# Performance work log

Hardware: AMD Instinct MI355X
Metric: run time of the kernel (lower is better)

Reference implementation:

```python
import jax, jax.numpy as jnp
import numpy as np

LN_EPS = 1e-5
B, N, D, V = 2048, 8, 1024, 4096


def setup_inputs() -> dict:
    key = jax.random.key(0)
    k1, k2, k3, k4 = jax.random.split(key, 4)
    return {
        "input_embedding": jax.random.normal(k1, (B, D), dtype=jnp.float32),
        "features": jax.random.randint(k2, (B, N), 0, V, dtype=jnp.int64),
        "embed_tables": jax.random.normal(k3, (N, V, D), dtype=jnp.float32) * 0.02,
        "W_pred": jax.random.normal(k4, (N, D, V), dtype=jnp.float32) * 0.02,
        "b_pred": jnp.zeros((N, V), dtype=jnp.float32),
        "ln_gamma": jnp.ones((D,), dtype=jnp.float32),
        "ln_beta": jnp.zeros((D,), dtype=jnp.float32),
    }


def reference(input_embedding, features, embed_tables, W_pred, b_pred, ln_gamma, ln_beta):
    # Per-feature embedding lookup: embed_tables[n, features[b,n]] -> [B, N, D]
    feat_emb = embed_tables[jnp.arange(N)[None, :], features]
    # Stack input embedding in front: [B, N+1, D]
    embeddings = jnp.concatenate([input_embedding[:, None, :], feat_emb], axis=1)
    # Original: triu(diag=1) mask-multiply-sum then [:, 1:, :].
    # masked_sums[:, t] = sum_{s < t} emb[:, s]; slicing t=1..N == inclusive cumsum
    # over the first N positions.
    masked_sums = jnp.cumsum(embeddings, axis=1)[:, :-1, :]  # [B, N, D]
    # LayerNorm over last dim
    mu = jnp.mean(masked_sums, axis=-1, keepdims=True)
    var = jnp.var(masked_sums, axis=-1, keepdims=True)
    h = (masked_sums - mu) / jnp.sqrt(var + LN_EPS) * ln_gamma + ln_beta
    # Exact (erf) GELU, matching nn.GELU default
    h = jax.nn.gelu(h, approximate=False)
    # Per-feature predictor heads as one batched GEMM: [B, N, V]
    logits = jnp.einsum("bnd,ndv->bnv", h, W_pred) + b_pred
    return logits
```

## Files before the change

kernel.cpp:

```cpp
#include <hip/hip_runtime.h>
#include <hip/hip_bf16.h>

#define B_ 2048
#define N_ 8
#define D_ 1024
#define V_ 4096
#define LN_EPS_ 1e-5f

typedef __bf16 bf16x8 __attribute__((ext_vector_type(8)));
typedef float f32x4 __attribute__((ext_vector_type(4)));

#define GLB(p) ((const __attribute__((address_space(1))) void*)(p))
#define LDSP(p) ((__attribute__((address_space(3))) void*)(p))

static __device__ __forceinline__ unsigned short f2bf(float x) {
    union { float f; unsigned int u; } v;
    v.f = x;
    unsigned int r = v.u + 0x7fffu + ((v.u >> 16) & 1u);
    return (unsigned short)(r >> 16);
}

__global__ __launch_bounds__(256) void prep(const float* __restrict__ ie,
                                            const int* __restrict__ feats,
                                            const float* __restrict__ emb,
                                            const float* __restrict__ gamma,
                                            const float* __restrict__ beta,
                                            const float* __restrict__ W,
                                            unsigned short* __restrict__ H,
                                            unsigned short* __restrict__ Wt) {
    const int bid = blockIdx.x;
    const int t = threadIdx.x;

    if (bid >= 2048) {
        __shared__ unsigned short tile[64][65];
        const int w  = bid - 2048;
        const int v0 = (w & 63) * 64;
        const int d0 = ((w >> 6) & 15) * 64;
        const int n  = w >> 10;
        const int tx = t & 15, ty = t >> 4;
#pragma unroll
        for (int i = 0; i < 4; ++i) {
            const int d = ty + i * 16;
            const float4 w4 = *(const float4*)&W[((size_t)n * D_ + d0 + d) * V_ + v0 + tx * 4];
            tile[d][tx * 4 + 0] = f2bf(w4.x);
            tile[d][tx * 4 + 1] = f2bf(w4.y);
            tile[d][tx * 4 + 2] = f2bf(w4.z);
            tile[d][tx * 4 + 3] = f2bf(w4.w);
        }
        __syncthreads();
#pragma unroll
        for (int i = 0; i < 4; ++i) {
            const int v = ty + i * 16;
            ushort4 pk;
            pk.x = tile[tx * 4 + 0][v];
            pk.y = tile[tx * 4 + 1][v];
            pk.z = tile[tx * 4 + 2][v];
            pk.w = tile[tx * 4 + 3][v];
            *reinterpret_cast<ushort4*>(&Wt[((size_t)n * V_ + v0 + v) * D_ + d0 + tx * 4]) = pk;
        }
    } else {
        __shared__ float redS[4], redQ[4];
        const int b = bid;
        const int d0 = t * 4;
        const int lane = t & 63, wid = t >> 6;

        float4 s  = *(const float4*)&ie[(size_t)b * D_ + d0];
        const float4 g4 = *(const float4*)&gamma[d0];
        const float4 be4 = *(const float4*)&beta[d0];

        int fc[N_];
#pragma unroll
        for (int n = 0; n < N_; ++n) fc[n] = feats[b * N_ + n];

#pragma unroll
        for (int n = 0; n < N_; ++n) {
            float ls = s.x + s.y + s.z + s.w;
            float lq = s.x * s.x + s.y * s.y + s.z * s.z + s.w * s.w;
#pragma unroll
            for (int off = 32; off > 0; off >>= 1) {
                ls += __shfl_down(ls, off, 64);
                lq += __shfl_down(lq, off, 64);
            }
            if (lane == 0) { redS[wid] = ls; redQ[wid] = lq; }
            __syncthreads();
            const float tot  = redS[0] + redS[1] + redS[2] + redS[3];
            const float totq = redQ[0] + redQ[1] + redQ[2] + redQ[3];
            __syncthreads();

            const float mu   = tot * (1.0f / D_);
            const float var  = totq * (1.0f / D_) - mu * mu;
            const float rstd = rsqrtf(var + LN_EPS_);

            float h0 = (s.x - mu) * rstd * g4.x + be4.x;
            float h1 = (s.y - mu) * rstd * g4.y + be4.y;
            float h2 = (s.z - mu) * rstd * g4.z + be4.z;
            float h3 = (s.w - mu) * rstd * g4.w + be4.w;
            h0 = 0.5f * h0 * (1.0f + erff(h0 * 0.70710678f));
            h1 = 0.5f * h1 * (1.0f + erff(h1 * 0.70710678f));
            h2 = 0.5f * h2 * (1.0f + erff(h2 * 0.70710678f));
            h3 = 0.5f * h3 * (1.0f + erff(h3 * 0.70710678f));

            ushort4 pk;
            pk.x = f2bf(h0); pk.y = f2bf(h1); pk.z = f2bf(h2); pk.w = f2bf(h3);
            *reinterpret_cast<ushort4*>(&H[((size_t)n * B_ + b) * D_ + d0]) = pk;

            const float4 e = *(const float4*)&emb[((size_t)n * V_ + fc[n]) * (size_t)D_ + d0];
            s.x += e.x; s.y += e.y; s.z += e.z; s.w += e.w;
        }
    }
}

#define MF(a, b, c) __builtin_amdgcn_mfma_f32_16x16x32_bf16((a), (b), (c), 0, 0, 0)

#define STG_A(u, kt, bb) __builtin_amdgcn_global_load_lds( \
    GLB(Ab + (size_t)((u) * 64 + srow) * D_ + (kt) + gsl), \
    LDSP(lds + (bb) + (u) * 8192 + t * 16), 16, 0, 0)
#define STG_B(u, kt, bb) __builtin_amdgcn_global_load_lds( \
    GLB(Bb + (size_t)((u) * 64 + srow) * D_ + (kt) + gsl), \
    LDSP(lds + (bb) + 32768 + (u) * 8192 + t * 16), 16, 0, 0)

#define RD_A(i, ks, bb) (*(const bf16x8*)(lds + (bb) + ((i) >> 1) * 8192 + \
    (((i) & 1) * 32 + wr * 16 + lrow) * 128 + ((((ks) * 4 + lkq) ^ sw) * 16)))
#define RD_B(j, ks, bb) (*(const bf16x8*)(lds + (bb) + 32768 + wc * 8192 + \
    ((j) * 16 + lrow) * 128 + ((((ks) * 4 + lkq) ^ sw) * 16)))

#define QUADP(i0, i1) \
    _Pragma("unroll") for (int j = 0; j < 4; ++j) { \
        acc[i0][j] = MF(A00, Bf[j][0], acc[i0][j]); \
        acc[i0][j] = MF(A01, Bf[j][1], acc[i0][j]); \
        acc[i1][j] = MF(A10, Bf[j][0], acc[i1][j]); \
        acc[i1][j] = MF(A11, Bf[j][1], acc[i1][j]); \
    }

#define TILE(KT, bc, bn) { \
    bf16x8 Bf[4][2]; \
    asm volatile("s_waitcnt vmcnt(3)" ::: "memory"); \
    __builtin_amdgcn_s_barrier(); \
    _Pragma("unroll") for (int j = 0; j < 4; ++j) { Bf[j][0] = RD_B(j, 0, bc); Bf[j][1] = RD_B(j, 1, bc); } \
    { bf16x8 A00 = RD_A(0, 0, bc), A01 = RD_A(0, 1, bc), A10 = RD_A(1, 0, bc), A11 = RD_A(1, 1, bc); \
      STG_B(0, (KT) + 64, bn); STG_B(1, (KT) + 64, bn); \
      __builtin_amdgcn_s_setprio(1); QUADP(0, 1); __builtin_amdgcn_s_setprio(0); } \
    __builtin_amdgcn_s_barrier(); \
    asm volatile("s_waitcnt vmcnt(4)" ::: "memory"); \
    __builtin_amdgcn_s_barrier(); \
    { bf16x8 A00 = RD_A(2, 0, bc), A01 = RD_A(2, 1, bc), A10 = RD_A(3, 0, bc), A11 = RD_A(3, 1, bc); \
      STG_B(2, (KT) + 64, bn); STG_B(3, (KT) + 64, bn); \
      __builtin_amdgcn_s_setprio(1); QUADP(2, 3); __builtin_amdgcn_s_setprio(0); } \
    __builtin_amdgcn_s_barrier(); \
    asm volatile("s_waitcnt vmcnt(4)" ::: "memory"); \
    __builtin_amdgcn_s_barrier(); \
    { bf16x8 A00 = RD_A(4, 0, bc), A01 = RD_A(4, 1, bc), A10 = RD_A(5, 0, bc), A11 = RD_A(5, 1, bc); \
      STG_A(0, (KT) + 64, bn); STG_A(1, (KT) + 64, bn); \
      __builtin_amdgcn_s_setprio(1); QUADP(4, 5); __builtin_amdgcn_s_setprio(0); } \
    __builtin_amdgcn_s_barrier(); \
    asm volatile("s_waitcnt vmcnt(6)" ::: "memory"); \
    __builtin_amdgcn_s_barrier(); \
    { bf16x8 A00 = RD_A(6, 0, bc), A01 = RD_A(6, 1, bc), A10 = RD_A(7, 0, bc), A11 = RD_A(7, 1, bc); \
      STG_A(2, (KT) + 64, bn); STG_A(3, (KT) + 64, bn); \
      __builtin_amdgcn_s_setprio(1); QUADP(6, 7); __builtin_amdgcn_s_setprio(0); } \
    __builtin_amdgcn_s_barrier(); \
}

#define TILE_LAST(bc) { \
    bf16x8 Bf[4][2]; \
    asm volatile("s_waitcnt vmcnt(3)" ::: "memory"); \
    __builtin_amdgcn_s_barrier(); \
    _Pragma("unroll") for (int j = 0; j < 4; ++j) { Bf[j][0] = RD_B(j, 0, bc); Bf[j][1] = RD_B(j, 1, bc); } \
    { bf16x8 A00 = RD_A(0, 0, bc), A01 = RD_A(0, 1, bc), A10 = RD_A(1, 0, bc), A11 = RD_A(1, 1, bc); \
      __builtin_amdgcn_s_setprio(1); QUADP(0, 1); __builtin_amdgcn_s_setprio(0); } \
    __builtin_amdgcn_s_barrier(); \
    asm volatile("s_waitcnt vmcnt(2)" ::: "memory"); \
    __builtin_amdgcn_s_barrier(); \
    { bf16x8 A00 = RD_A(2, 0, bc), A01 = RD_A(2, 1, bc), A10 = RD_A(3, 0, bc), A11 = RD_A(3, 1, bc); \
      __builtin_amdgcn_s_setprio(1); QUADP(2, 3); __builtin_amdgcn_s_setprio(0); } \
    __builtin_amdgcn_s_barrier(); \
    asm volatile("s_waitcnt vmcnt(1)" ::: "memory"); \
    __builtin_amdgcn_s_barrier(); \
    { bf16x8 A00 = RD_A(4, 0, bc), A01 = RD_A(4, 1, bc), A10 = RD_A(5, 0, bc), A11 = RD_A(5, 1, bc); \
      __builtin_amdgcn_s_setprio(1); QUADP(4, 5); __builtin_amdgcn_s_setprio(0); } \
    __builtin_amdgcn_s_barrier(); \
    asm volatile("s_waitcnt vmcnt(0)" ::: "memory"); \
    __builtin_amdgcn_s_barrier(); \
    { bf16x8 A00 = RD_A(6, 0, bc), A01 = RD_A(6, 1, bc), A10 = RD_A(7, 0, bc), A11 = RD_A(7, 1, bc); \
      __builtin_amdgcn_s_setprio(1); QUADP(6, 7); __builtin_amdgcn_s_setprio(0); } \
}

__global__ __launch_bounds__(512, 2) void gemm8(const unsigned short* __restrict__ H,
                                                const unsigned short* __restrict__ Wt,
                                                const float* __restrict__ bp,
                                                float* __restrict__ out) {
    extern __shared__ char lds[];
    const int vt = blockIdx.x, mt = blockIdx.y, n = blockIdx.z;
    const int t = threadIdx.x;
    const int wid = t >> 6, lane = t & 63;
    const int wr = wid >> 2, wc = wid & 3;

    const unsigned short* Ab = H  + ((size_t)n * B_ + (size_t)mt * 256) * D_;
    const unsigned short* Bb = Wt + ((size_t)n * V_ + (size_t)vt * 256) * D_;

    const int srow = t >> 3;
    const int gsl  = ((t & 7) ^ (srow & 7)) * 8;
    const int lrow = lane & 15;
    const int lkq  = lane >> 4;
    const int sw   = lane & 7;

    const int col = lane & 15;
    float bias[4];
#pragma unroll
    for (int j = 0; j < 4; ++j)
        bias[j] = bp[(size_t)n * V_ + vt * 256 + wc * 64 + j * 16 + col];
    asm volatile("s_waitcnt vmcnt(0)" ::: "memory");
    __builtin_amdgcn_sched_barrier(0);

    f32x4 acc[8][4] = {};

    STG_B(0, 0, 0); STG_B(1, 0, 0); STG_B(2, 0, 0); STG_B(3, 0, 0);
    STG_A(0, 0, 0); STG_A(1, 0, 0); STG_A(2, 0, 0); STG_A(3, 0, 0);

    int kt = 0;
#pragma unroll 1
    for (int it = 0; it < 7; ++it) {
        TILE(kt, 0, 65536); kt += 64;
        TILE(kt, 65536, 0); kt += 64;
    }
    TILE(kt, 0, 65536);
    TILE_LAST(65536);

    const int rg  = (lane >> 4) * 4;
    const int gc0 = vt * 256 + wc * 64 + col;
#pragma unroll
    for (int i = 0; i < 8; ++i) {
        const int row = mt * 256 + i * 32 + wr * 16 + rg;
#pragma unroll
        for (int j = 0; j < 4; ++j) {
            const int gcol = gc0 + j * 16;
#pragma unroll
            for (int r = 0; r < 4; ++r) {
                out[((size_t)(row + r) * N_ + n) * V_ + gcol] = acc[i][j][r] + bias[j];
            }
        }
    }
}

extern "C" void kernel_launch(void* const* d_in, const int* in_sizes, int n_in,
                              void* d_out, int out_size, void* d_ws, size_t ws_size,
                              hipStream_t stream) {
    const float* ie  = (const float*)d_in[0];
    const int*   fts = (const int*)d_in[1];
    const float* emb = (const float*)d_in[2];
    const float* W   = (const float*)d_in[3];
    const float* bp  = (const float*)d_in[4];
    const float* gam = (const float*)d_in[5];
    const float* bet = (const float*)d_in[6];
    float* out = (float*)d_out;

    unsigned short* Wt = (unsigned short*)d_ws;
    unsigned short* H  = (unsigned short*)((char*)d_ws + (size_t)N_ * V_ * D_ * 2);

    (void)hipFuncSetAttribute(reinterpret_cast<const void*>(gemm8),
                              hipFuncAttributeMaxDynamicSharedMemorySize, 131072);

    prep<<<dim3(2048 + 8192), dim3(256), 0, stream>>>(ie, fts, emb, gam, bet, W, H, Wt);
    gemm8<<<dim3(V_ / 256, B_ / 256, N_), dim3(512), 131072, stream>>>(H, Wt, bp, out);
}
```

Measured before the change: 232.4 us.

## Switch GEMM to 32x32x16 MFMA with MFMA-native pre-tiled operand layouts

Result: no change. 235.3 us (+1.2%).

```diff
diff --git a/kernel.cpp b/kernel.cpp
--- a/kernel.cpp
+++ b/kernel.cpp
@@ -8,7 +8,7 @@
 #define LN_EPS_ 1e-5f
 
 typedef __bf16 bf16x8 __attribute__((ext_vector_type(8)));
-typedef float f32x4 __attribute__((ext_vector_type(4)));
+typedef float f32x16 __attribute__((ext_vector_type(16)));
 
 #define GLB(p) ((const __attribute__((address_space(1))) void*)(p))
 #define LDSP(p) ((__attribute__((address_space(3))) void*)(p))
@@ -19,6 +19,7 @@
     unsigned int r = v.u + 0x7fffu + ((v.u >> 16) & 1u);
     return (unsigned short)(r >> 16);
 }
+
 
 __global__ __launch_bounds__(256) void prep(const float* __restrict__ ie,
                                             const int* __restrict__ feats,
@@ -49,14 +50,24 @@
         }
         __syncthreads();
 #pragma unroll
-        for (int i = 0; i < 4; ++i) {
-            const int v = ty + i * 16;
-            ushort4 pk;
-            pk.x = tile[tx * 4 + 0][v];
-            pk.y = tile[tx * 4 + 1][v];
-            pk.z = tile[tx * 4 + 2][v];
-            pk.w = tile[tx * 4 + 3][v];
-            *reinterpret_cast<ushort4*>(&Wt[((size_t)n * V_ + v0 + v) * D_ + d0 + tx * 4]) = pk;
+        for (int p = 0; p < 2; ++p) {
+            const int g   = t + p * 256;
+            const int c   = g & 31;
+            const int cbl = (g >> 5) & 1;
+            const int kq  = g >> 6;
+            ushort4 lo, hi;
+            lo.x = tile[kq * 8 + 0][cbl * 32 + c];
+            lo.y = tile[kq * 8 + 1][cbl * 32 + c];
+            lo.z = tile[kq * 8 + 2][cbl * 32 + c];
+            lo.w = tile[kq * 8 + 3][cbl * 32 + c];
+            hi.x = tile[kq * 8 + 4][cbl * 32 + c];
+            hi.y = tile[kq * 8 + 5][cbl * 32 + c];
+            hi.z = tile[kq * 8 + 6][cbl * 32 + c];
+            hi.w = tile[kq * 8 + 7][cbl * 32 + c];
+            const size_t goff = (size_t)n * 4194304 + (size_t)((v0 >> 5) + cbl) * 32768
+                              + (size_t)((d0 >> 3) + kq) * 256 + c * 8;
+            *reinterpret_cast<ushort4*>(&Wt[goff])     = lo;
+            *reinterpret_cast<ushort4*>(&Wt[goff + 4]) = hi;
         }
     } else {
         __shared__ float redS[4], redQ[4];
@@ -71,6 +82,9 @@
         int fc[N_];
 #pragma unroll
         for (int n = 0; n < N_; ++n) fc[n] = feats[b * N_ + n];
+
+        const size_t hbase = (size_t)(b >> 5) * 32768 + (size_t)(t >> 1) * 256
+                           + (b & 31) * 8 + (t & 1) * 4;
 
 #pragma unroll
         for (int n = 0; n < N_; ++n) {
@@ -102,7 +116,7 @@
 
             ushort4 pk;
             pk.x = f2bf(h0); pk.y = f2bf(h1); pk.z = f2bf(h2); pk.w = f2bf(h3);
-            *reinterpret_cast<ushort4*>(&H[((size_t)n * B_ + b) * D_ + d0]) = pk;
+            *reinterpret_cast<ushort4*>(&H[(size_t)n * 2097152 + hbase]) = pk;
 
             const float4 e = *(const float4*)&emb[((size_t)n * V_ + fc[n]) * (size_t)D_ + d0];
             s.x += e.x; s.y += e.y; s.z += e.z; s.w += e.w;
@@ -110,133 +124,131 @@
     }
 }
 
-#define MF(a, b, c) __builtin_amdgcn_mfma_f32_16x16x32_bf16((a), (b), (c), 0, 0, 0)
-
-#define STG_A(u, kt, bb) __builtin_amdgcn_global_load_lds( \
-    GLB(Ab + (size_t)((u) * 64 + srow) * D_ + (kt) + gsl), \
-    LDSP(lds + (bb) + (u) * 8192 + t * 16), 16, 0, 0)
-#define STG_B(u, kt, bb) __builtin_amdgcn_global_load_lds( \
-    GLB(Bb + (size_t)((u) * 64 + srow) * D_ + (kt) + gsl), \
-    LDSP(lds + (bb) + 32768 + (u) * 8192 + t * 16), 16, 0, 0)
-
-#define RD_A(i, ks, bb) (*(const bf16x8*)(lds + (bb) + ((i) >> 1) * 8192 + \
-    (((i) & 1) * 32 + wr * 16 + lrow) * 128 + ((((ks) * 4 + lkq) ^ sw) * 16)))
-#define RD_B(j, ks, bb) (*(const bf16x8*)(lds + (bb) + 32768 + wc * 8192 + \
-    ((j) * 16 + lrow) * 128 + ((((ks) * 4 + lkq) ^ sw) * 16)))
-
-#define QUADP(i0, i1) \
-    _Pragma("unroll") for (int j = 0; j < 4; ++j) { \
-        acc[i0][j] = MF(A00, Bf[j][0], acc[i0][j]); \
-        acc[i0][j] = MF(A01, Bf[j][1], acc[i0][j]); \
-        acc[i1][j] = MF(A10, Bf[j][0], acc[i1][j]); \
-        acc[i1][j] = MF(A11, Bf[j][1], acc[i1][j]); \
-    }
-
-#define TILE(KT, bc, bn) { \
-    bf16x8 Bf[4][2]; \
+#define MF32(a, b, c) __builtin_amdgcn_mfma_f32_32x32x16_bf16((a), (b), (c), 0, 0, 0)
+
+#define STG_A(u, KTQ, bb) __builtin_amdgcn_global_load_lds( \
+    GLB(Ab + (u) * 65536 + (KTQ) * 256), LDSP(lds + (bb) + (u) * 8192 + t * 16), 16, 0, 0)
+#define STG_B(u, KTQ, bb) __builtin_amdgcn_global_load_lds( \
+    GLB(Bb + (u) * 65536 + (KTQ) * 256), LDSP(lds + (bb) + 32768 + (u) * 8192 + t * 16), 16, 0, 0)
+
+#define RD_A32(p, ks, bb) (*(const bf16x8*)(lds + (bb) + (p) * 8192 + wr * 4096 + ((ks) * 2 + h) * 512 + l31 * 16))
+#define RD_B32(j, ks, bb) (*(const bf16x8*)(lds + (bb) + 32768 + wc * 8192 + (j) * 4096 + ((ks) * 2 + h) * 512 + l31 * 16))
+
+#define MMP(p) \
+    acc[p][0] = MF32(Af[0], Bf0[0], acc[p][0]); acc[p][1] = MF32(Af[0], Bf1[0], acc[p][1]); \
+    acc[p][0] = MF32(Af[1], Bf0[1], acc[p][0]); acc[p][1] = MF32(Af[1], Bf1[1], acc[p][1]); \
+    acc[p][0] = MF32(Af[2], Bf0[2], acc[p][0]); acc[p][1] = MF32(Af[2], Bf1[2], acc[p][1]); \
+    acc[p][0] = MF32(Af[3], Bf0[3], acc[p][0]); acc[p][1] = MF32(Af[3], Bf1[3], acc[p][1]);
+
+#define TILE32(bc, bn, KTQN) { \
+    bf16x8 Bf0[4], Bf1[4], Af[4]; \
     asm volatile("s_waitcnt vmcnt(3)" ::: "memory"); \
     __builtin_amdgcn_s_barrier(); \
-    _Pragma("unroll") for (int j = 0; j < 4; ++j) { Bf[j][0] = RD_B(j, 0, bc); Bf[j][1] = RD_B(j, 1, bc); } \
-    { bf16x8 A00 = RD_A(0, 0, bc), A01 = RD_A(0, 1, bc), A10 = RD_A(1, 0, bc), A11 = RD_A(1, 1, bc); \
-      STG_B(0, (KT) + 64, bn); STG_B(1, (KT) + 64, bn); \
-      __builtin_amdgcn_s_setprio(1); QUADP(0, 1); __builtin_amdgcn_s_setprio(0); } \
+    _Pragma("unroll") for (int ks = 0; ks < 4; ++ks) { Bf0[ks] = RD_B32(0, ks, bc); Bf1[ks] = RD_B32(1, ks, bc); } \
+    _Pragma("unroll") for (int ks = 0; ks < 4; ++ks) Af[ks] = RD_A32(0, ks, bc); \
+    STG_B(0, KTQN, bn); STG_B(1, KTQN, bn); \
+    __builtin_amdgcn_s_setprio(1); MMP(0); __builtin_amdgcn_s_setprio(0); \
     __builtin_amdgcn_s_barrier(); \
     asm volatile("s_waitcnt vmcnt(4)" ::: "memory"); \
     __builtin_amdgcn_s_barrier(); \
-    { bf16x8 A00 = RD_A(2, 0, bc), A01 = RD_A(2, 1, bc), A10 = RD_A(3, 0, bc), A11 = RD_A(3, 1, bc); \
-      STG_B(2, (KT) + 64, bn); STG_B(3, (KT) + 64, bn); \
-      __builtin_amdgcn_s_setprio(1); QUADP(2, 3); __builtin_amdgcn_s_setprio(0); } \
+    _Pragma("unroll") for (int ks = 0; ks < 4; ++ks) Af[ks] = RD_A32(1, ks, bc); \
+    STG_B(2, KTQN, bn); STG_B(3, KTQN, bn); \
+    __builtin_amdgcn_s_setprio(1); MMP(1); __builtin_amdgcn_s_setprio(0); \
     __builtin_amdgcn_s_barrier(); \
     asm volatile("s_waitcnt vmcnt(4)" ::: "memory"); \
     __builtin_amdgcn_s_barrier(); \
-    { bf16x8 A00 = RD_A(4, 0, bc), A01 = RD_A(4, 1, bc), A10 = RD_A(5, 0, bc), A11 = RD_A(5, 1, bc); \
-      STG_A(0, (KT) + 64, bn); STG_A(1, (KT) + 64, bn); \
-      __builtin_amdgcn_s_setprio(1); QUADP(4, 5); __builtin_amdgcn_s_setprio(0); } \
+    _Pragma("unroll") for (int ks = 0; ks < 4; ++ks) Af[ks] = RD_A32(2, ks, bc); \
+    STG_A(0, KTQN, bn); STG_A(1, KTQN, bn); \
+    __builtin_amdgcn_s_setprio(1); MMP(2); __builtin_amdgcn_s_setprio(0); \
     __builtin_amdgcn_s_barrier(); \
     asm volatile("s_waitcnt vmcnt(6)" ::: "memory"); \
     __builtin_amdgcn_s_barrier(); \
-    { bf16x8 A00 = RD_A(6, 0, bc), A01 = RD_A(6, 1, bc), A10 = RD_A(7, 0, bc), A11 = RD_A(7, 1, bc); \
-      STG_A(2, (KT) + 64, bn); STG_A(3, (KT) + 64, bn); \
-      __builtin_amdgcn_s_setprio(1); QUADP(6, 7); __builtin_amdgcn_s_setprio(0); } \
-    __builtin_amdgcn_s_barrier(); \
-}
-
-#define TILE_LAST(bc) { \
-    bf16x8 Bf[4][2]; \
+    _Pragma("unroll") for (int ks = 0; ks < 4; ++ks) Af[ks] = RD_A32(3, ks, bc); \
+    STG_A(2, KTQN, bn); STG_A(3, KTQN, bn); \
+    __builtin_amdgcn_s_setprio(1); MMP(3); __builtin_amdgcn_s_setprio(0); \
+    __builtin_amdgcn_s_barrier(); \
+}
+
+#define TILE32_LAST(bc) { \
+    bf16x8 Bf0[4], Bf1[4], Af[4]; \
     asm volatile("s_waitcnt vmcnt(3)" ::: "memory"); \
     __builtin_amdgcn_s_barrier(); \
-    _Pragma("unroll") for (int j = 0; j < 4; ++j) { Bf[j][0] = RD_B(j, 0, bc); Bf[j][1] = RD_B(j, 1, bc); } \
-    { bf16x8 A00 = RD_A(0, 0, bc), A01 = RD_A(0, 1, bc), A10 = RD_A(1, 0, bc), A11 = RD_A(1, 1, bc); \
-      __builtin_amdgcn_s_setprio(1); QUADP(0, 1); __builtin_amdgcn_s_setprio(0); } \
+    _Pragma("unroll") for (int ks = 0; ks < 4; ++ks) { Bf0[ks] = RD_B32(0, ks, bc); Bf1[ks] = RD_B32(1, ks, bc); } \
+    _Pragma("unroll") for (int ks = 0; ks < 4; ++ks) Af[ks] = RD_A32(0, ks, bc); \
+    __builtin_amdgcn_s_setprio(1); MMP(0); __builtin_amdgcn_s_setprio(0); \
     __builtin_amdgcn_s_barrier(); \
     asm volatile("s_waitcnt vmcnt(2)" ::: "memory"); \
     __builtin_amdgcn_s_barrier(); \
-    { bf16x8 A00 = RD_A(2, 0, bc), A01 = RD_A(2, 1, bc), A10 = RD_A(3, 0, bc), A11 = RD_A(3, 1, bc); \
-      __builtin_amdgcn_s_setprio(1); QUADP(2, 3); __builtin_amdgcn_s_setprio(0); } \
+    _Pragma("unroll") for (int ks = 0; ks < 4; ++ks) Af[ks] = RD_A32(1, ks, bc); \
+    __builtin_amdgcn_s_setprio(1); MMP(1); __builtin_amdgcn_s_setprio(0); \
     __builtin_amdgcn_s_barrier(); \
     asm volatile("s_waitcnt vmcnt(1)" ::: "memory"); \
     __builtin_amdgcn_s_barrier(); \
-    { bf16x8 A00 = RD_A(4, 0, bc), A01 = RD_A(4, 1, bc), A10 = RD_A(5, 0, bc), A11 = RD_A(5, 1, bc); \
-      __builtin_amdgcn_s_setprio(1); QUADP(4, 5); __builtin_amdgcn_s_setprio(0); } \
+    _Pragma("unroll") for (int ks = 0; ks < 4; ++ks) Af[ks] = RD_A32(2, ks, bc); \
+    __builtin_amdgcn_s_setprio(1); MMP(2); __builtin_amdgcn_s_setprio(0); \
     __builtin_amdgcn_s_barrier(); \
     asm volatile("s_waitcnt vmcnt(0)" ::: "memory"); \
     __builtin_amdgcn_s_barrier(); \
-    { bf16x8 A00 = RD_A(6, 0, bc), A01 = RD_A(6, 1, bc), A10 = RD_A(7, 0, bc), A11 = RD_A(7, 1, bc); \
-      __builtin_amdgcn_s_setprio(1); QUADP(6, 7); __builtin_amdgcn_s_setprio(0); } \
-}
-
-__global__ __launch_bounds__(512, 2) void gemm8(const unsigned short* __restrict__ H,
-                                                const unsigned short* __restrict__ Wt,
-                                                const float* __restrict__ bp,
-                                                float* __restrict__ out) {
+    _Pragma("unroll") for (int ks = 0; ks < 4; ++ks) Af[ks] = RD_A32(3, ks, bc); \
+    __builtin_amdgcn_s_setprio(1); MMP(3); __builtin_amdgcn_s_setprio(0); \
+}
+
+__global__ __launch_bounds__(512, 2) void gemm32(const unsigned short* __restrict__ H,
+                                                 const unsigned short* __restrict__ Wt,
+                                                 const float* __restrict__ bp,
+                                                 float* __restrict__ out) {
     extern __shared__ char lds[];
-    const int vt = blockIdx.x, mt = blockIdx.y, n = blockIdx.z;
+    const int bid = blockIdx.x;
+    const int logical = (bid & 7) * 128 + (bid >> 3);
+    const int n  = logical >> 7;
+    const int mt = (logical >> 4) & 7;
+    const int vt = logical & 15;
+
     const int t = threadIdx.x;
     const int wid = t >> 6, lane = t & 63;
     const int wr = wid >> 2, wc = wid & 3;
-
-    const unsigned short* Ab = H  + ((size_t)n * B_ + (size_t)mt * 256) * D_;
-    const unsigned short* Bb = Wt + ((size_t)n * V_ + (size_t)vt * 256) * D_;
-
-    const int srow = t >> 3;
-    const int gsl  = ((t & 7) ^ (srow & 7)) * 8;
-    const int lrow = lane & 15;
-    const int lkq  = lane >> 4;
-    const int sw   = lane & 7;
-
-    const int col = lane & 15;
-    float bias[4];
-#pragma unroll
-    for (int j = 0; j < 4; ++j)
-        bias[j] = bp[(size_t)n * V_ + vt * 256 + wc * 64 + j * 16 + col];
+    const int h = lane >> 5, l31 = lane & 31;
+
+    const unsigned short* Ab = H  + (size_t)n * 2097152 + (size_t)mt * 262144
+                             + (t >> 8) * 32768 + ((t >> 5) & 7) * 256 + (t & 31) * 8;
+    const unsigned short* Bb = Wt + (size_t)n * 4194304 + (size_t)vt * 262144
+                             + (t >> 8) * 32768 + ((t >> 5) & 7) * 256 + (t & 31) * 8;
+
+    float bias[2];
+#pragma unroll
+    for (int j = 0; j < 2; ++j)
+        bias[j] = bp[(size_t)n * V_ + vt * 256 + wc * 64 + j * 32 + l31];
     asm volatile("s_waitcnt vmcnt(0)" ::: "memory");
     __builtin_amdgcn_sched_barrier(0);
 
-    f32x4 acc[8][4] = {};
+    f32x16 acc[4][2];
+#pragma unroll
+    for (int p = 0; p < 4; ++p)
+#pragma unroll
+        for (int r = 0; r < 16; ++r) { acc[p][0][r] = 0.f; acc[p][1][r] = 0.f; }
 
     STG_B(0, 0, 0); STG_B(1, 0, 0); STG_B(2, 0, 0); STG_B(3, 0, 0);
     STG_A(0, 0, 0); STG_A(1, 0, 0); STG_A(2, 0, 0); STG_A(3, 0, 0);
 
-    int kt = 0;
+    int ktq = 0;
 #pragma unroll 1
     for (int it = 0; it < 7; ++it) {
-        TILE(kt, 0, 65536); kt += 64;
-        TILE(kt, 65536, 0); kt += 64;
+        TILE32(0, 65536, ktq + 8);  ktq += 8;
+        TILE32(65536, 0, ktq + 8);  ktq += 8;
     }
-    TILE(kt, 0, 65536);
-    TILE_LAST(65536);
-
-    const int rg  = (lane >> 4) * 4;
-    const int gc0 = vt * 256 + wc * 64 + col;
-#pragma unroll
-    for (int i = 0; i < 8; ++i) {
-        const int row = mt * 256 + i * 32 + wr * 16 + rg;
-#pragma unroll
-        for (int j = 0; j < 4; ++j) {
-            const int gcol = gc0 + j * 16;
-#pragma unroll
-            for (int r = 0; r < 4; ++r) {
-                out[((size_t)(row + r) * N_ + n) * V_ + gcol] = acc[i][j][r] + bias[j];
+    TILE32(0, 65536, 120);
+    TILE32_LAST(65536);
+
+    const int gc0 = vt * 256 + wc * 64 + l31;
+#pragma unroll
+    for (int p = 0; p < 4; ++p) {
+#pragma unroll
+        for (int j = 0; j < 2; ++j) {
+            const int gcol = gc0 + j * 32;
+#pragma unroll
+            for (int r = 0; r < 16; ++r) {
+                const int row = mt * 256 + p * 64 + wr * 32 + (r & 3) + 8 * (r >> 2) + 4 * h;
+                out[((size_t)row * N_ + n) * V_ + gcol] = acc[p][j][r] + bias[j];
             }
         }
     }
@@ -257,9 +269,9 @@
     unsigned short* Wt = (unsigned short*)d_ws;
     unsigned short* H  = (unsigned short*)((char*)d_ws + (size_t)N_ * V_ * D_ * 2);
 
-    (void)hipFuncSetAttribute(reinterpret_cast<const void*>(gemm8),
+    (void)hipFuncSetAttribute(reinterpret_cast<const void*>(gemm32),
                               hipFuncAttributeMaxDynamicSharedMemorySize, 131072);
 
     prep<<<dim3(2048 + 8192), dim3(256), 0, stream>>>(ie, fts, emb, gam, bet, W, H, Wt);
-    gemm8<<<dim3(V_ / 256, B_ / 256, N_), dim3(512), 131072, stream>>>(H, Wt, bp, out);
-}
+    gemm32<<<dim3(1024), dim3(512), 131072, stream>>>(H, Wt, bp, out);
+}
```
